# Optimization experiments

Hardware: AMD Instinct MI355X
Metric: run time of the kernel (lower is better)

The kernel has to match this reference:

```python
import jax, jax.numpy as jnp
import numpy as np

D_MODEL = 1024
NUM_HEADS = 16
HEAD_DIM = D_MODEL // NUM_HEADS
SCALE = 1.0 / np.sqrt(HEAD_DIM).astype(np.float32)


def setup_inputs() -> dict:
    key = jax.random.key(0)
    k1, k2, k3, k4 = jax.random.split(key, 4)
    B, L = 1, 4096
    s = 0.02
    x = jax.random.normal(k1, (B, L, D_MODEL), dtype=jnp.float32)
    W_qkv = jax.random.normal(k2, (D_MODEL, 3 * D_MODEL), dtype=jnp.float32) * s
    W_o = jax.random.normal(k3, (D_MODEL, D_MODEL), dtype=jnp.float32) * s
    b_o = jax.random.normal(k4, (D_MODEL,), dtype=jnp.float32) * s
    return {"x": x, "W_qkv": W_qkv, "W_o": W_o, "b_o": b_o}


def reference(x, W_qkv, W_o, b_o):
    B, L, D = x.shape
    H, Hd = NUM_HEADS, HEAD_DIM
    qkv = x @ W_qkv                          # [B, L, 3D]
    qkv = qkv.reshape(B, L, 3, H, Hd)
    q = jnp.transpose(qkv[:, :, 0], (0, 2, 1, 3))  # [B, H, L, Hd]
    k = jnp.transpose(qkv[:, :, 1], (0, 2, 1, 3))
    v = jnp.transpose(qkv[:, :, 2], (0, 2, 1, 3))
    scores = jnp.einsum("bhqd,bhkd->bhqk", q, k) * SCALE  # [B, H, L, L]
    attn = jax.nn.softmax(scores, axis=-1)
    out = jnp.einsum("bhqk,bhkd->bhqd", attn, v)          # [B, H, L, Hd]
    out = jnp.transpose(out, (0, 2, 1, 3)).reshape(B, L, D)
    return out @ W_o + b_o
```

## Files before the change

### kernel.cpp

```cpp
#include <hip/hip_runtime.h>
#include <stdint.h>


#define L_SEQ 4096
#define DM 1024
#define NHEAD 16
#define HDIM 64
#define ATT_SCALE 0.125f
#define LOG2E 1.4426950408889634f
#define CSC (ATT_SCALE * LOG2E)

typedef __attribute__((ext_vector_type(8))) __bf16 bf16x8;
typedef __attribute__((ext_vector_type(4))) __bf16 bf16x4;
typedef __attribute__((ext_vector_type(4))) float f32x4;
typedef __attribute__((ext_vector_type(8))) float f32x8;
typedef __attribute__((ext_vector_type(4))) short short4v;
typedef __attribute__((ext_vector_type(8))) short short8v;

#define GLL16(g, l) __builtin_amdgcn_global_load_lds( \
    (__attribute__((address_space(1))) void*)(g),     \
    (__attribute__((address_space(3))) void*)(l), 16, 0, 0)

#define MFMA32(a, b, c) __builtin_amdgcn_mfma_f32_16x16x32_bf16((a), (b), (c), 0, 0, 0)

__device__ __forceinline__ short f2bf(float f) {
  uint32_t u = __builtin_bit_cast(uint32_t, f);
  u += 0x7fffu + ((u >> 16) & 1u);
  return (short)(u >> 16);
}

__global__ __launch_bounds__(256)
void prep_kernel(const float* __restrict__ x, short* __restrict__ xb,
                 const float* __restrict__ Wq, short* __restrict__ wqt,
                 const float* __restrict__ Wo, short* __restrict__ wot) {
  __shared__ __align__(16) short tbuf[64 * 66];
  const int tid = threadIdx.x;
  const int blk = blockIdx.x;
  if (blk < 4096) {
    int i = blk * 256 + tid;
    float4 v = ((const float4*)x)[i];
    short4 o;
    o.x = f2bf(v.x); o.y = f2bf(v.y); o.z = f2bf(v.z); o.w = f2bf(v.w);
    ((short4*)xb)[i] = o;
    return;
  }
  const float* W; short* Wt; int N, nb, kb;
  const int K = 1024;
  if (blk < 4096 + 768) {
    int b = blk - 4096;
    W = Wq; Wt = wqt; N = 3072; nb = (b % 48) * 64; kb = (b / 48) * 64;
  } else {
    int b = blk - (4096 + 768);
    W = Wo; Wt = wot; N = 1024; nb = (b % 16) * 64; kb = (b / 16) * 64;
  }
#pragma unroll
  for (int i = 0; i < 16; i++) {
    int idx = tid + i * 256;
    int r = idx >> 6, c = idx & 63;
    tbuf[r * 66 + c] = f2bf(W[(size_t)(kb + r) * N + nb + c]);
  }
  __syncthreads();
#pragma unroll
  for (int i = 0; i < 16; i++) {
    int idx = tid + i * 256;
    int r = idx >> 6, c = idx & 63;
    Wt[(size_t)(nb + r) * K + kb + c] = tbuf[c * 66 + r];
  }
}

__global__ __launch_bounds__(256, 2)
void gemm_qkv(const short* __restrict__ A, const short* __restrict__ Bt,
              short* __restrict__ qkv, short* __restrict__ vtout, int K) {
  __shared__ __align__(16) short As[4096];
  __shared__ __align__(16) short Bs[4096];
  const int tid = threadIdx.x;
  const int lane = tid & 63;
  const int wave = tid >> 6;
  const int quad = lane >> 4;
  const int cl = lane & 15;
  const int m0 = blockIdx.x * 128;
  const int n0 = blockIdx.y * 128;
  const int wm = (wave >> 1) * 64;
  const int wn = (wave & 1) * 64;

  f32x4 acc[4][4] = {};

  for (int kb = 0; kb < K; kb += 32) {
    __syncthreads();
#pragma unroll
    for (int i = 0; i < 2; i++) {
      int ci = i * 256 + tid;
      int row = ci & 127, c = ci >> 7;
      GLL16(A + (size_t)(m0 + row) * K + kb + c * 8, As + ci * 8);
      GLL16(Bt + (size_t)(n0 + row) * K + kb + c * 8, Bs + ci * 8);
    }
    __syncthreads();
    bf16x8 af[4], bfr[4];
#pragma unroll
    for (int t = 0; t < 4; t++) {
      af[t]  = *(const bf16x8*)(As + (quad * 128 + wm + t * 16 + cl) * 8);
      bfr[t] = *(const bf16x8*)(Bs + (quad * 128 + wn + t * 16 + cl) * 8);
    }
#pragma unroll
    for (int mt = 0; mt < 4; mt++)
#pragma unroll
      for (int nt = 0; nt < 4; nt++)
        acc[mt][nt] = MFMA32(af[mt], bfr[nt], acc[mt][nt]);
  }

#pragma unroll
  for (int mt = 0; mt < 4; mt++)
#pragma unroll
    for (int nt = 0; nt < 4; nt++) {
      int col = n0 + wn + nt * 16 + cl;
      int which = col >> 10, hd = col & 63;
      int hidx = (col >> 6) & 15;
      int row0 = m0 + wm + mt * 16 + quad * 4;
      if (which == 2) {
        short4v pk;
#pragma unroll
        for (int r = 0; r < 4; r++) pk[r] = f2bf(acc[mt][nt][r]);
        *(short4v*)(vtout + ((size_t)hidx * HDIM + hd) * L_SEQ + row0) = pk;
      } else {
        float sc = (which == 0) ? CSC : 1.0f;
        size_t base = (((size_t)which * NHEAD + hidx) * L_SEQ) * HDIM + hd;
#pragma unroll
        for (int r = 0; r < 4; r++)
          qkv[base + (size_t)(row0 + r) * HDIM] = f2bf(acc[mt][nt][r] * sc);
      }
    }
}

__global__ __launch_bounds__(256, 2)
void gemm_out(const short* __restrict__ A, const short* __restrict__ Bt,
              float* __restrict__ C, const float* __restrict__ bias, int K) {
  __shared__ __align__(16) short As[4096];
  __shared__ __align__(16) short Bs[2048];
  const int tid = threadIdx.x;
  const int lane = tid & 63;
  const int wave = tid >> 6;
  const int quad = lane >> 4;
  const int cl = lane & 15;
  const int m0 = blockIdx.x * 128;
  const int n0 = blockIdx.y * 64;
  const int wm = (wave >> 1) * 64;
  const int wn = (wave & 1) * 32;
  const int N = 1024;

  f32x4 acc[4][2] = {};

  for (int kb = 0; kb < K; kb += 32) {
    __syncthreads();
#pragma unroll
    for (int i = 0; i < 2; i++) {
      int ci = i * 256 + tid;
      GLL16(A + (size_t)(m0 + (ci & 127)) * K + kb + (ci >> 7) * 8, As + ci * 8);
    }
    GLL16(Bt + (size_t)(n0 + (tid & 63)) * K + kb + (tid >> 6) * 8, Bs + tid * 8);
    __syncthreads();
    bf16x8 af[4], bfr[2];
#pragma unroll
    for (int t = 0; t < 4; t++)
      af[t] = *(const bf16x8*)(As + (quad * 128 + wm + t * 16 + cl) * 8);
#pragma unroll
    for (int t = 0; t < 2; t++)
      bfr[t] = *(const bf16x8*)(Bs + (quad * 64 + wn + t * 16 + cl) * 8);
#pragma unroll
    for (int mt = 0; mt < 4; mt++)
#pragma unroll
      for (int nt = 0; nt < 2; nt++)
        acc[mt][nt] = MFMA32(af[mt], bfr[nt], acc[mt][nt]);
  }

#pragma unroll
  for (int mt = 0; mt < 4; mt++)
#pragma unroll
    for (int nt = 0; nt < 2; nt++) {
      int col = n0 + wn + nt * 16 + cl;
      float b = bias[col];
#pragma unroll
      for (int r = 0; r < 4; r++) {
        int row = m0 + wm + mt * 16 + quad * 4 + r;
        C[(size_t)row * N + col] = acc[mt][nt][r] + b;
      }
    }
}

__global__ __launch_bounds__(256, 4)
void attn_kernel(const short* __restrict__ qkv, const short* __restrict__ vt,
                 short* __restrict__ aout) {
  __shared__ __align__(16) short Ks[2][4096];
  __shared__ __align__(16) short Vs[2][4096];
  const int tid = threadIdx.x, lane = tid & 63, wave = tid >> 6;
  const int quad = lane >> 4, cl = lane & 15;
  const int bid = blockIdx.x;
  const int h  = ((bid & 7) << 1) | ((bid >> 3) & 1);
  const int qb = bid >> 4;
  const short* Qg = qkv + (size_t)h * L_SEQ * HDIM;
  const short* Kg = qkv + ((size_t)NHEAD + h) * L_SEQ * HDIM;
  const short* Vg = vt + (size_t)h * HDIM * L_SEQ;
  const int keyoff = ((cl >> 2) << 3) | (cl & 3);

  bf16x8 qf[2];
  {
    int qrow = qb * 64 + wave * 16 + cl;
    qf[0] = *(const bf16x8*)(Qg + (size_t)qrow * HDIM + quad * 8);
    qf[1] = *(const bf16x8*)(Qg + (size_t)qrow * HDIM + 32 + quad * 8);
  }
  const short8v ov = {0x3F80, 0x3F80, 0x3F80, 0x3F80, 0x3F80, 0x3F80, 0x3F80, 0x3F80};
  const bf16x8 ones = __builtin_bit_cast(bf16x8, ov);
  f32x4 o_l = {};
  f32x4 o_acc[4] = {};

  int koff[2][2][2];
  int voff[2][4];
#pragma unroll
  for (int kslab = 0; kslab < 2; kslab++) {
#pragma unroll
    for (int b = 0; b < 2; b++) {
      int krow = kslab * 32 + keyoff + b * 4;
      int sw = (krow & 3) | (((krow >> 3) & 1) << 2);
#pragma unroll
      for (int ks = 0; ks < 2; ks++)
        koff[kslab][b][ks] = (krow * 8 + ((ks * 4 + quad) ^ sw)) * 8;
    }
#pragma unroll
    for (int G = 0; G < 4; G++) {
      int vrow = G * 16 + cl;
      int sw = (vrow & 3) | (((vrow >> 3) & 1) << 2);
      voff[kslab][G] = (vrow * 8 + ((kslab * 4 + quad) ^ sw)) * 8;
    }
  }

  const short* kp[2]; const short* vp[2]; int ldso[2];
#pragma unroll
  for (int i = 0; i < 2; i++) {
    int ci = i * 256 + tid;
    int row = ci >> 3;
    int sw = (row & 3) | (((row >> 3) & 1) << 2);
    int c = (ci & 7) ^ sw;
    kp[i] = Kg + (size_t)row * HDIM + c * 8;
    vp[i] = Vg + (size_t)row * L_SEQ + c * 8;
    ldso[i] = ci * 8;
  }
#define STAGE(t, buf)                                       \
  {                                                         \
    _Pragma("unroll")                                       \
    for (int i = 0; i < 2; i++) {                           \
      GLL16(kp[i] + (t) * 64 * HDIM, &Ks[buf][ldso[i]]);    \
      GLL16(vp[i] + (t) * 64, &Vs[buf][ldso[i]]);           \
    }                                                       \
  }

  STAGE(0, 0);
#pragma unroll 2
  for (int t = 0; t < L_SEQ / 64; t++) {
    const int cur = t & 1;
    __syncthreads();
    if (t + 1 < L_SEQ / 64) STAGE(t + 1, cur ^ 1);
    const short* Kb = Ks[cur];
    const short* Vb = Vs[cur];

    f32x4 s[2][2] = {};
    __builtin_amdgcn_s_setprio(1);
#pragma unroll
    for (int kslab = 0; kslab < 2; kslab++)
#pragma unroll
      for (int b = 0; b < 2; b++)
#pragma unroll
        for (int ks = 0; ks < 2; ks++) {
          bf16x8 kf = *(const bf16x8*)(Kb + koff[kslab][b][ks]);
          s[kslab][b] = MFMA32(kf, qf[ks], s[kslab][b]);
        }
    __builtin_amdgcn_s_setprio(0);

    bf16x8 vfr0[4], vfr1[4];
#pragma unroll
    for (int G = 0; G < 4; G++)
      vfr0[G] = *(const bf16x8*)(Vb + voff[0][G]);

    bf16x8 pb0;
    {
      f32x8 pv8;
#pragma unroll
      for (int b = 0; b < 2; b++)
#pragma unroll
        for (int r = 0; r < 4; r++)
          pv8[b * 4 + r] = __builtin_amdgcn_exp2f(s[0][b][r]);
      pb0 = __builtin_convertvector(pv8, bf16x8);
    }

#pragma unroll
    for (int G = 0; G < 4; G++)
      vfr1[G] = *(const bf16x8*)(Vb + voff[1][G]);

    __builtin_amdgcn_s_setprio(1);
    o_l = MFMA32(ones, pb0, o_l);
#pragma unroll
    for (int G = 0; G < 4; G++)
      o_acc[G] = MFMA32(vfr0[G], pb0, o_acc[G]);
    __builtin_amdgcn_s_setprio(0);

    bf16x8 pb1;
    {
      f32x8 pv8;
#pragma unroll
      for (int b = 0; b < 2; b++)
#pragma unroll
        for (int r = 0; r < 4; r++)
          pv8[b * 4 + r] = __builtin_amdgcn_exp2f(s[1][b][r]);
      pb1 = __builtin_convertvector(pv8, bf16x8);
    }

    __builtin_amdgcn_s_setprio(1);
    o_l = MFMA32(ones, pb1, o_l);
#pragma unroll
    for (int G = 0; G < 4; G++)
      o_acc[G] = MFMA32(vfr1[G], pb1, o_acc[G]);
    __builtin_amdgcn_s_setprio(0);
  }
#undef STAGE

  {
    float inv = 1.f / o_l[0];
    int token = qb * 64 + wave * 16 + cl;
#pragma unroll
    for (int G = 0; G < 4; G++) {
      f32x4 sc = o_acc[G] * inv;
      bf16x4 pk = __builtin_convertvector(sc, bf16x4);
      *(short4v*)(aout + (size_t)token * DM + h * HDIM + G * 16 + quad * 4) =
          __builtin_bit_cast(short4v, pk);
    }
  }
}

extern "C" void kernel_launch(void* const* d_in, const int* in_sizes, int n_in,
                              void* d_out, int out_size, void* d_ws, size_t ws_size,
                              hipStream_t stream) {
  const float* x    = (const float*)d_in[0];
  const float* Wqkv = (const float*)d_in[1];
  const float* Wo   = (const float*)d_in[2];
  const float* bo   = (const float*)d_in[3];
  char* ws = (char*)d_ws;
  short* xb    = (short*)(ws);
  short* wqkvt = (short*)(ws + (size_t)8 * 1024 * 1024);
  short* wot   = (short*)(ws + (size_t)14 * 1024 * 1024);
  short* qkv   = (short*)(ws + (size_t)16 * 1024 * 1024);
  short* vt    = (short*)(ws + (size_t)40 * 1024 * 1024);
  short* aout  = xb;
  float* out = (float*)d_out;

  prep_kernel<<<4096 + 768 + 256, 256, 0, stream>>>(x, xb, Wqkv, wqkvt, Wo, wot);
  gemm_qkv<<<dim3(32, 24), 256, 0, stream>>>(xb, wqkvt, qkv, vt, DM);
  attn_kernel<<<dim3(1024), 256, 0, stream>>>(qkv, vt, aout);
  gemm_out<<<dim3(32, 16), 256, 0, stream>>>(aout, wot, out, bo, DM);
}
```

Before: 246.1 us.

## Split attention waves into key and query groups with LDS reduction of partial outputs

Each wave now handles 32 queries and half of each 64-key tile (a 2x2 split of key groups and query groups), instead of 16 queries over all 64 keys. Each K and V fragment read from LDS is reused across two query subtiles, which halves the LDS fragment reads per MFMA. The two key-group partial outputs and row sums are combined at the end through shared memory. The cost is more accumulator registers per wave and an extra reduction step with two barriers.

```diff
diff --git a/kernel.cpp b/kernel.cpp
--- a/kernel.cpp
+++ b/kernel.cpp
@@ -193,6 +193,8 @@
   __shared__ __align__(16) short Vs[2][4096];
   const int tid = threadIdx.x, lane = tid & 63, wave = tid >> 6;
   const int quad = lane >> 4, cl = lane & 15;
+  const int kg = wave >> 1;
+  const int qg = wave & 1;
   const int bid = blockIdx.x;
   const int h  = ((bid & 7) << 1) | ((bid >> 3) & 1);
   const int qb = bid >> 4;
@@ -201,35 +203,33 @@
   const short* Vg = vt + (size_t)h * HDIM * L_SEQ;
   const int keyoff = ((cl >> 2) << 3) | (cl & 3);
 
-  bf16x8 qf[2];
-  {
-    int qrow = qb * 64 + wave * 16 + cl;
-    qf[0] = *(const bf16x8*)(Qg + (size_t)qrow * HDIM + quad * 8);
-    qf[1] = *(const bf16x8*)(Qg + (size_t)qrow * HDIM + 32 + quad * 8);
+  bf16x8 qf[2][2];
+#pragma unroll
+  for (int qs = 0; qs < 2; qs++) {
+    int qrow = qb * 64 + qg * 32 + qs * 16 + cl;
+    qf[qs][0] = *(const bf16x8*)(Qg + (size_t)qrow * HDIM + quad * 8);
+    qf[qs][1] = *(const bf16x8*)(Qg + (size_t)qrow * HDIM + 32 + quad * 8);
   }
   const short8v ov = {0x3F80, 0x3F80, 0x3F80, 0x3F80, 0x3F80, 0x3F80, 0x3F80, 0x3F80};
   const bf16x8 ones = __builtin_bit_cast(bf16x8, ov);
-  f32x4 o_l = {};
-  f32x4 o_acc[4] = {};
-
-  int koff[2][2][2];
-  int voff[2][4];
-#pragma unroll
-  for (int kslab = 0; kslab < 2; kslab++) {
-#pragma unroll
-    for (int b = 0; b < 2; b++) {
-      int krow = kslab * 32 + keyoff + b * 4;
-      int sw = (krow & 3) | (((krow >> 3) & 1) << 2);
-#pragma unroll
-      for (int ks = 0; ks < 2; ks++)
-        koff[kslab][b][ks] = (krow * 8 + ((ks * 4 + quad) ^ sw)) * 8;
-    }
-#pragma unroll
-    for (int G = 0; G < 4; G++) {
-      int vrow = G * 16 + cl;
-      int sw = (vrow & 3) | (((vrow >> 3) & 1) << 2);
-      voff[kslab][G] = (vrow * 8 + ((kslab * 4 + quad) ^ sw)) * 8;
-    }
+  f32x4 o_l[2] = {};
+  f32x4 o_acc[4][2] = {};
+
+  int koff[2][2];
+#pragma unroll
+  for (int b = 0; b < 2; b++) {
+    int krow = kg * 32 + keyoff + b * 4;
+    int sw = (krow & 3) | (((krow >> 3) & 1) << 2);
+#pragma unroll
+    for (int ks = 0; ks < 2; ks++)
+      koff[b][ks] = (krow * 8 + ((ks * 4 + quad) ^ sw)) * 8;
+  }
+  int voff[4];
+#pragma unroll
+  for (int G = 0; G < 4; G++) {
+    int vrow = G * 16 + cl;
+    int sw = (vrow & 3) | (((vrow >> 3) & 1) << 2);
+    voff[G] = (vrow * 8 + ((kg * 4 + quad) ^ sw)) * 8;
   }
 
   const short* kp[2]; const short* vp[2]; int ldso[2];
@@ -264,20 +264,20 @@
     f32x4 s[2][2] = {};
     __builtin_amdgcn_s_setprio(1);
 #pragma unroll
-    for (int kslab = 0; kslab < 2; kslab++)
-#pragma unroll
-      for (int b = 0; b < 2; b++)
-#pragma unroll
-        for (int ks = 0; ks < 2; ks++) {
-          bf16x8 kf = *(const bf16x8*)(Kb + koff[kslab][b][ks]);
-          s[kslab][b] = MFMA32(kf, qf[ks], s[kslab][b]);
-        }
+    for (int b = 0; b < 2; b++)
+#pragma unroll
+      for (int ks = 0; ks < 2; ks++) {
+        bf16x8 kf = *(const bf16x8*)(Kb + koff[b][ks]);
+#pragma unroll
+        for (int qs = 0; qs < 2; qs++)
+          s[qs][b] = MFMA32(kf, qf[qs][ks], s[qs][b]);
+      }
     __builtin_amdgcn_s_setprio(0);
 
-    bf16x8 vfr0[4], vfr1[4];
+    bf16x8 vfr[4];
 #pragma unroll
     for (int G = 0; G < 4; G++)
-      vfr0[G] = *(const bf16x8*)(Vb + voff[0][G]);
+      vfr[G] = *(const bf16x8*)(Vb + voff[G]);
 
     bf16x8 pb0;
     {
@@ -290,15 +290,11 @@
       pb0 = __builtin_convertvector(pv8, bf16x8);
     }
 
+    __builtin_amdgcn_s_setprio(1);
+    o_l[0] = MFMA32(ones, pb0, o_l[0]);
 #pragma unroll
     for (int G = 0; G < 4; G++)
-      vfr1[G] = *(const bf16x8*)(Vb + voff[1][G]);
-
-    __builtin_amdgcn_s_setprio(1);
-    o_l = MFMA32(ones, pb0, o_l);
-#pragma unroll
-    for (int G = 0; G < 4; G++)
-      o_acc[G] = MFMA32(vfr0[G], pb0, o_acc[G]);
+      o_acc[G][0] = MFMA32(vfr[G], pb0, o_acc[G][0]);
     __builtin_amdgcn_s_setprio(0);
 
     bf16x8 pb1;
@@ -313,23 +309,42 @@
     }
 
     __builtin_amdgcn_s_setprio(1);
-    o_l = MFMA32(ones, pb1, o_l);
+    o_l[1] = MFMA32(ones, pb1, o_l[1]);
 #pragma unroll
     for (int G = 0; G < 4; G++)
-      o_acc[G] = MFMA32(vfr1[G], pb1, o_acc[G]);
+      o_acc[G][1] = MFMA32(vfr[G], pb1, o_acc[G][1]);
     __builtin_amdgcn_s_setprio(0);
   }
 #undef STAGE
 
-  {
-    float inv = 1.f / o_l[0];
-    int token = qb * 64 + wave * 16 + cl;
-#pragma unroll
-    for (int G = 0; G < 4; G++) {
-      f32x4 sc = o_acc[G] * inv;
-      bf16x4 pk = __builtin_convertvector(sc, bf16x4);
-      *(short4v*)(aout + (size_t)token * DM + h * HDIM + G * 16 + quad * 4) =
-          __builtin_bit_cast(short4v, pk);
+  __syncthreads();
+  float* ored = (float*)&Ks[0][0];
+  float* lred = (float*)&Vs[0][0];
+  if (kg == 1) {
+#pragma unroll
+    for (int G = 0; G < 4; G++)
+#pragma unroll
+      for (int qs = 0; qs < 2; qs++)
+        *(f32x4*)&ored[(((qg * 4 + G) * 2 + qs) * 64 + lane) * 4] = o_acc[G][qs];
+#pragma unroll
+    for (int qs = 0; qs < 2; qs++)
+      lred[(qg * 2 + qs) * 64 + lane] = o_l[qs][0];
+  }
+  __syncthreads();
+  if (kg == 0) {
+#pragma unroll
+    for (int qs = 0; qs < 2; qs++) {
+      float l = o_l[qs][0] + lred[(qg * 2 + qs) * 64 + lane];
+      float inv = 1.f / l;
+      int token = qb * 64 + qg * 32 + qs * 16 + cl;
+#pragma unroll
+      for (int G = 0; G < 4; G++) {
+        f32x4 part = *(const f32x4*)&ored[(((qg * 4 + G) * 2 + qs) * 64 + lane) * 4];
+        f32x4 sc = (o_acc[G][qs] + part) * inv;
+        bf16x4 pk = __builtin_convertvector(sc, bf16x4);
+        *(short4v*)(aout + (size_t)token * DM + h * HDIM + G * 16 + quad * 4) =
+            __builtin_bit_cast(short4v, pk);
+      }
     }
   }
 }
```

Result: no change. 243.6 us (-1.0%).
